# Kernel tuning notes

Measured on AMD Instinct MI355X. Metric: run time of the kernel, lower is better.

## Reference

```python
import jax, jax.numpy as jnp
import numpy as np

SAMPLE_RATE = 16000
SOUND_SPEED = 343.0
MAX_ORDER = 15
RIR_LENGTH = 3968
WINDOW_LENGTH = 81
PAD = WINDOW_LENGTH // 2  # 40

# Static image-source lattice (depends only on max_order): all integer
# reflection index triplets with |nx|+|ny|+|nz| <= max_order.
_ind = np.arange(-MAX_ORDER, MAX_ORDER + 1)
_grid = np.stack(np.meshgrid(_ind, _ind, _ind, indexing="ij"), -1).reshape(-1, 3)
XYZ = _grid[np.abs(_grid).sum(1) <= MAX_ORDER].astype(np.float32)  # (I,3), I=4991
EXP_LO = np.abs(np.floor(XYZ / 2)).astype(np.float32)        # hits on lower walls per dim
EXP_HI = np.abs(np.floor((XYZ + 1) / 2)).astype(np.float32)  # hits on upper walls per dim


def _hann(x, T):
    # continuous Hann window sampled at non-integer points, zero outside |x|<=T/2
    return jnp.where(jnp.abs(x) <= T / 2, 0.5 * (1.0 + jnp.cos(2.0 * jnp.pi * x / T)), 0.0)


def _forward(inp):
    room = inp[:, 0:3]                 # (B,3) room dimensions [m]
    mic = inp[:, 3:6] * room           # (B,3)
    src = inp[:, 6:9] * room           # (B,3)
    a_w = inp[:, 9:10]
    absorption = jnp.concatenate([a_w, a_w, a_w, a_w, inp[:, 10:11], inp[:, 11:12]], axis=1)
    absorption = absorption * 0.84 + 0.01            # (B,6): [x-,x+,y-,y+,floor,ceiling]
    tr = jnp.sqrt(1.0 - absorption)                  # wall reflection coefficients

    xyz = jnp.asarray(XYZ)                           # (I,3)
    d = room[:, None, :]
    s = src[:, None, :]
    # image source locations (B,I,3): mirror parity per torchaudio ISM
    img_loc = jnp.where(xyz % 2 == 1, d * (xyz + 1.0) - s, d * xyz + s)
    # per-image-source attenuation (B,I)
    t_lo = tr[:, None, 0::2]                         # (B,1,3) lower walls per dim
    t_hi = tr[:, None, 1::2]                         # (B,1,3) upper walls per dim
    att = jnp.prod(t_lo ** jnp.asarray(EXP_LO) * t_hi ** jnp.asarray(EXP_HI), axis=-1)

    dist = jnp.linalg.norm(img_loc - mic[:, None, :], axis=-1)   # (B,I)
    amp = att / dist                                              # 1/r spreading
    delay = dist * (SAMPLE_RATE / SOUND_SPEED)                    # fractional sample delay
    delay_i = jnp.ceil(delay)

    # windowed-sinc fractional-delay pulse sampled at n = delay_i-PAD .. delay_i+PAD
    n_rel = jnp.arange(-PAD, PAD + 1, dtype=jnp.float32)          # (W,)
    x = delay_i[..., None] + n_rel - delay[..., None]             # (B,I,W)
    sig = amp[..., None] * jnp.sinc(x) * _hann(x, 2 * PAD)        # (B,I,W)

    # scatter-accumulate pulses at time index n, dropping out-of-range samples
    t_idx = (delay_i[..., None] + n_rel).astype(jnp.int32)        # (B,I,W)
    B = inp.shape[0]
    b_idx = jnp.arange(B, dtype=jnp.int32)[:, None, None]
    rir = jnp.zeros((B, RIR_LENGTH), dtype=sig.dtype).at[b_idx, t_idx].add(sig, mode="drop")

    toa = PAD + SAMPLE_RATE * jnp.linalg.norm(mic - src, axis=1) / SOUND_SPEED  # (B,)
    return rir, toa


def setup_inputs():
    key = jax.random.key(0)
    u = jax.random.uniform(key, (128, 12), dtype=jnp.float32)
    room = 2.0 + 8.0 * u[:, :3]          # room dims in [2,10] m
    rest = 0.05 + 0.9 * u[:, 3:]         # mic/src fractions and absorptions in (0,1)
    return {"input": jnp.concatenate([room, rest], axis=1)}


def reference(input):
    return _forward(input)
```

## Files before the change

### kernel.cpp

```cpp
#include <hip/hip_runtime.h>

#define NIMG    4991
#define RIRLEN  3968
#define NT      512
#define NGRP    16
#define CAP     2048
#define KPT     10
#define INV_PI  0.31830988618379067f
#define SR_OVER_C 46.647230320699704f

struct Tab { int v[NIMG]; };
static constexpr Tab make_tab() {
    Tab t{};
    int k = 0;
    for (int x = -15; x <= 15; ++x)
        for (int y = -15; y <= 15; ++y)
            for (int z = -15; z <= 15; ++z) {
                int ax = x < 0 ? -x : x;
                int ay = y < 0 ? -y : y;
                int az = z < 0 ? -z : z;
                if (ax + ay + az <= 15)
                    t.v[k++] = (x + 15) | ((y + 15) << 8) | ((z + 15) << 16);
            }
    return t;
}
__constant__ Tab c_tab = make_tab();

static __device__ __forceinline__ int iabs(int v) { return v < 0 ? -v : v; }
static __device__ __forceinline__ int imin(int a, int b) { return a < b ? a : b; }

typedef __fp16 f16x2 __attribute__((ext_vector_type(2)));

__global__ __launch_bounds__(NT, 8)
void rir_fused(const float* __restrict__ inp, float* __restrict__ out, int B) {
    const int bx   = blockIdx.x;
    const int b    = bx >> 4;
    const int g    = bx & 15;
    const int tid  = threadIdx.x;
    const int lane = tid & 63;
    const int wv   = tid >> 6;
    const int q    = lane & 3;

    __shared__ __align__(16) float2   s_dh[CAP];
    __shared__ __align__(16) unsigned s_cs[CAP];
    __shared__ float    s_par[12];
    __shared__ float    s_p2[3][32];
    __shared__ float    s_at[3][32];
    __shared__ int      s_h4[256][4];
    __shared__ int      s_off[257];
    __shared__ float    s_acc[4][64];

    for (int k = tid; k < 1024; k += NT) ((int*)s_h4)[k] = 0;
    if (tid < 256) ((float*)s_acc)[tid] = 0.0f;
    if (tid == 0) {
        const float* ip = inp + b * 12;
        float rx = ip[0], ry = ip[1], rz = ip[2];
        float mx = ip[3] * rx, my = ip[4] * ry, mz = ip[5] * rz;
        float sx = ip[6] * rx, sy = ip[7] * ry, sz = ip[8] * rz;
        float aw = __builtin_fmaf(ip[9],  0.84f, 0.01f);
        float a4 = __builtin_fmaf(ip[10], 0.84f, 0.01f);
        float a5 = __builtin_fmaf(ip[11], 0.84f, 0.01f);
        s_par[0] = rx; s_par[1] = ry; s_par[2] = rz;
        s_par[3] = mx; s_par[4] = my; s_par[5] = mz;
        s_par[6] = sx; s_par[7] = sy; s_par[8] = sz;
        s_par[9]  = 0.5f * __builtin_amdgcn_logf(1.0f - aw);
        s_par[10] = 0.5f * __builtin_amdgcn_logf(1.0f - a4);
        s_par[11] = 0.5f * __builtin_amdgcn_logf(1.0f - a5);
        if (g == 0) {
            float dx = mx - sx, dy = my - sy, dz = mz - sz;
            out[(size_t)B * RIRLEN + b] = __builtin_fmaf(
                __builtin_sqrtf(dx * dx + dy * dy + dz * dz), SR_OVER_C, 40.0f);
        }
    }
    __syncthreads();

    if (tid < 96) {
        const int axis = tid >> 5;
        const int j    = tid & 31;
        if (j < 31) {
            const int n = j - 15;
            const float rr = s_par[axis];
            const float mm = s_par[3 + axis];
            const float ss = s_par[6 + axis];
            const float iv = (n & 1) ? __builtin_fmaf(rr, (float)(n + 1), -ss)
                                     : __builtin_fmaf(rr, (float)n, ss);
            const float pv = iv - mm;
            s_p2[axis][j] = pv * pv;
            const float e4 = (float)iabs(n >> 1);
            const float e5 = (float)iabs((n + 1) >> 1);
            const float ex = (axis < 2)
                ? (e4 + e5) * s_par[9]
                : __builtin_fmaf(e4, s_par[10], e5 * s_par[11]);
            s_at[axis][j] = __builtin_amdgcn_exp2f(ex);
        }
    }
    __syncthreads();

    const int fb = 4 * g + 1;

    float2   edh[KPT];
    unsigned ecs[KPT];
    int      enc[KPT];
    #pragma unroll
    for (int k = 0; k < KPT; ++k) {
        enc[k] = -1;
        const int idx = tid + k * NT;
        if (idx < NIMG) {
            const int p  = c_tab.v[idx];
            const int xi = p & 255;
            const int yi = (p >> 8) & 255;
            const int zi = (p >> 16) & 255;
            const float d2   = s_p2[0][xi] + s_p2[1][yi] + s_p2[2][zi];
            const float dist = __builtin_sqrtf(d2);
            const float delay = dist * SR_OVER_C;
            const float di    = __builtin_ceilf(delay);
            const int   ti0   = (int)di - 40;
            const int   bk    = (ti0 + 96) >> 4;
            const bool owned  = ((unsigned)((bk - fb + 64) & 63) < 9u);
            if (ti0 < RIRLEN && owned) {
                const float att = s_at[0][xi] * s_at[1][yi] * s_at[2][zi];
                const float amp = att * __builtin_amdgcn_rcpf(dist);
                float frac = di - delay;
                if (frac == 0.0f) frac = di * 1.52587890625e-05f;
                const int dii = (int)di;
                float c1p = amp * __builtin_amdgcn_sinf(0.5f * frac) * INV_PI;
                if (dii & 1) c1p = -c1p;
                const float Hp     = 0.5f * c1p;
                const float dstore = di - frac;
                const float rv = dstore * 0.0125f;
                const float fr = rv - __builtin_floorf(rv);
                const float Hcd = Hp * __builtin_amdgcn_cosf(fr);
                const float Hsd = Hp * __builtin_amdgcn_sinf(fr);
                const f16x2 pk2 = __builtin_amdgcn_cvt_pkrtz(Hcd, Hsd);

                const int rnk = atomicAdd(&s_h4[bk][q], 1);
                enc[k] = (bk << 13) | rnk;
                edh[k] = make_float2(dstore, Hp);
                ecs[k] = __builtin_bit_cast(unsigned, pk2);
            }
        }
    }
    __syncthreads();

    if (wv == 0) {
        const int l = lane;
        const int4 a0 = *(const int4*)&s_h4[4 * l + 0][0];
        const int4 a1 = *(const int4*)&s_h4[4 * l + 1][0];
        const int4 a2 = *(const int4*)&s_h4[4 * l + 2][0];
        const int4 a3 = *(const int4*)&s_h4[4 * l + 3][0];
        const int c0 = a0.x + a0.y + a0.z + a0.w;
        const int c1 = a1.x + a1.y + a1.z + a1.w;
        const int c2 = a2.x + a2.y + a2.z + a2.w;
        const int c3 = a3.x + a3.y + a3.z + a3.w;
        const int ts = c0 + c1 + c2 + c3;
        int incl = ts;
        #pragma unroll
        for (int d = 1; d < 64; d <<= 1) {
            const int u = __shfl_up(incl, d, 64);
            if (l >= d) incl += u;
        }
        const int base = incl - ts;
        s_off[4 * l + 0] = imin(base, CAP);
        s_off[4 * l + 1] = imin(base + c0, CAP);
        s_off[4 * l + 2] = imin(base + c0 + c1, CAP);
        s_off[4 * l + 3] = imin(base + c0 + c1 + c2, CAP);
        if (l == 63) s_off[256] = imin(incl, CAP);
    }
    __syncthreads();

    if (tid < 256) {
        int run = s_off[tid];
        #pragma unroll
        for (int p = 0; p < 4; ++p) {
            const int c = s_h4[tid][p];
            s_h4[tid][p] = run;
            run += c;
        }
    }
    __syncthreads();

    #pragma unroll
    for (int k = 0; k < KPT; ++k) {
        if (enc[k] >= 0) {
            const int bk   = enc[k] >> 13;
            const int slot = s_h4[bk][q] + (enc[k] & 8191);
            if (slot < CAP) {
                s_dh[slot] = edh[k];
                s_cs[slot] = ecs[k];
            }
        }
    }
    __syncthreads();

    int wlo[4], wlen[4], wpre[4];
    int T = 0, nw = 0;
    #pragma unroll
    for (int kk = 0; kk < 4; ++kk) {
        const int wi = g + 16 * kk;
        wpre[kk] = T;
        if (wi < 62) {
            wlo[kk]  = s_off[4 * wi + 1];
            wlen[kk] = s_off[4 * wi + 10] - wlo[kk];
            T += wlen[kk];
            nw = kk + 1;
        } else { wlo[kk] = 0; wlen[kk] = 0; }
    }
    const int a0r = (T * wv) >> 3;
    const int a1r = (T * (wv + 1)) >> 3;

#define EV1(ACC, DLY, HPV, PKU) do {                                         \
        const f16x2 hh = __builtin_bit_cast(f16x2, (PKU));                   \
        const float xw = tf - (DLY);                                         \
        const float pre = __builtin_fmaf(cth0, (float)hh.x,                  \
                              __builtin_fmaf(sth0, (float)hh.y, (HPV)));     \
        const float hm = (__builtin_fabsf(xw) <= 40.0f) ? pre : 0.0f;        \
        ACC = __builtin_fmaf(hm, __builtin_amdgcn_rcpf(xw), ACC);            \
    } while (0)

    #pragma unroll
    for (int kk = 0; kk < 4; ++kk) {
        if (wlen[kk] == 0) continue;
        const int o0 = (wpre[kk] > a0r) ? wpre[kk] : a0r;
        const int oe = ((wpre[kk] + wlen[kk]) < a1r) ? (wpre[kk] + wlen[kk]) : a1r;
        if (o0 >= oe) continue;
        int       i  = wlo[kk] + (o0 - wpre[kk]);
        const int ie = wlo[kk] + (oe - wpre[kk]);

        const int   wi   = g + 16 * kk;
        const int   t    = (wi << 6) + lane;
        const float tf   = (float)t;
        const int   m    = t - (t / 80) * 80;
        const float cth0 = __builtin_amdgcn_cosf((float)m * 0.0125f);
        const float sth0 = __builtin_amdgcn_sinf((float)m * 0.0125f);

        float acc0 = 0.0f, acc1 = 0.0f;
        while (i < ie && (i & 3)) { EV1(acc0, s_dh[i].x, s_dh[i].y, s_cs[i]); ++i; }
        for (; i + 4 <= ie; i += 4) {
            const float4 d0 = *(const float4*)&s_dh[i];
            const float4 d1 = *(const float4*)&s_dh[i + 2];
            const uint4  cc = *(const uint4*)&s_cs[i];
            EV1(acc0, d0.x, d0.y, cc.x); EV1(acc1, d0.z, d0.w, cc.y);
            EV1(acc0, d1.x, d1.y, cc.z); EV1(acc1, d1.z, d1.w, cc.w);
        }
        for (; i < ie; ++i) EV1(acc0, s_dh[i].x, s_dh[i].y, s_cs[i]);

        atomicAdd(&s_acc[kk][lane], acc0 + acc1);
    }
#undef EV1
    __syncthreads();

    if (tid < 64 * nw) {
        const int kk = tid >> 6;
        const int wi = g + 16 * kk;
        const int t  = (wi << 6) + lane;
        const float sl = (lane & 1) ? -1.0f : 1.0f;
        out[(size_t)b * RIRLEN + t] = sl * s_acc[kk][lane];
    }
}

extern "C" void kernel_launch(void* const* d_in, const int* in_sizes, int n_in,
                              void* d_out, int out_size, void* d_ws, size_t ws_size,
                              hipStream_t stream) {
    (void)d_ws; (void)ws_size; (void)n_in; (void)out_size;
    const float* inp = (const float*)d_in[0];
    float* out = (float*)d_out;
    const int B = in_sizes[0] / 12;
    rir_fused<<<dim3(B * NGRP), dim3(NT), 0, stream>>>(inp, out, B);
}
```

Measured before the change: 103.1 us.

## Split fused RIR kernel into per-batch prep and per-group gather kernels

The fused kernel had each of 16 groups per batch item recompute all ~5000 image sources, bin them and prefix-sum them, keeping only the ones it owns. The new path runs a prep kernel once per batch item that computes, bins and writes sorted image-source data plus offsets to workspace. A gather kernel then loads each group's slice into shared memory and evaluates the windowed-sinc sum. This removes the 16x redundant source computation but adds a second launch and a global-memory round trip. It falls back to the fused kernel when the workspace is too small.

```diff
diff --git a/kernel.cpp b/kernel.cpp
--- a/kernel.cpp
+++ b/kernel.cpp
@@ -28,8 +28,259 @@
 
 static __device__ __forceinline__ int iabs(int v) { return v < 0 ? -v : v; }
 static __device__ __forceinline__ int imin(int a, int b) { return a < b ? a : b; }
+static __device__ __forceinline__ int imax(int a, int b) { return a > b ? a : b; }
 
 typedef __fp16 f16x2 __attribute__((ext_vector_type(2)));
+
+
+__global__ __launch_bounds__(NT)
+void rir_prep(const float* __restrict__ inp, float* __restrict__ out,
+              float2* __restrict__ wdh, unsigned* __restrict__ wcs,
+              int* __restrict__ offs, int B) {
+    const int b    = blockIdx.x;
+    const int tid  = threadIdx.x;
+    const int lane = tid & 63;
+    const int wv   = tid >> 6;
+    const int q    = lane & 3;
+
+    __shared__ float s_par[12];
+    __shared__ float s_p2[3][32];
+    __shared__ float s_at[3][32];
+    __shared__ int   s_h4[256][4];
+    __shared__ int   s_off[257];
+
+    for (int k = tid; k < 1024; k += NT) ((int*)s_h4)[k] = 0;
+    if (tid == 0) {
+        const float* ip = inp + b * 12;
+        float rx = ip[0], ry = ip[1], rz = ip[2];
+        float mx = ip[3] * rx, my = ip[4] * ry, mz = ip[5] * rz;
+        float sx = ip[6] * rx, sy = ip[7] * ry, sz = ip[8] * rz;
+        float aw = __builtin_fmaf(ip[9],  0.84f, 0.01f);
+        float a4 = __builtin_fmaf(ip[10], 0.84f, 0.01f);
+        float a5 = __builtin_fmaf(ip[11], 0.84f, 0.01f);
+        s_par[0] = rx; s_par[1] = ry; s_par[2] = rz;
+        s_par[3] = mx; s_par[4] = my; s_par[5] = mz;
+        s_par[6] = sx; s_par[7] = sy; s_par[8] = sz;
+        s_par[9]  = 0.5f * __builtin_amdgcn_logf(1.0f - aw);
+        s_par[10] = 0.5f * __builtin_amdgcn_logf(1.0f - a4);
+        s_par[11] = 0.5f * __builtin_amdgcn_logf(1.0f - a5);
+        float dx = mx - sx, dy = my - sy, dz = mz - sz;
+        out[(size_t)B * RIRLEN + b] = __builtin_fmaf(
+            __builtin_sqrtf(dx * dx + dy * dy + dz * dz), SR_OVER_C, 40.0f);
+    }
+    __syncthreads();
+
+    if (tid < 96) {
+        const int axis = tid >> 5;
+        const int j    = tid & 31;
+        if (j < 31) {
+            const int n = j - 15;
+            const float rr = s_par[axis];
+            const float mm = s_par[3 + axis];
+            const float ss = s_par[6 + axis];
+            const float iv = (n & 1) ? __builtin_fmaf(rr, (float)(n + 1), -ss)
+                                     : __builtin_fmaf(rr, (float)n, ss);
+            const float pv = iv - mm;
+            s_p2[axis][j] = pv * pv;
+            const float e4 = (float)iabs(n >> 1);
+            const float e5 = (float)iabs((n + 1) >> 1);
+            const float ex = (axis < 2)
+                ? (e4 + e5) * s_par[9]
+                : __builtin_fmaf(e4, s_par[10], e5 * s_par[11]);
+            s_at[axis][j] = __builtin_amdgcn_exp2f(ex);
+        }
+    }
+    __syncthreads();
+
+    float2   edh[KPT];
+    unsigned ecs[KPT];
+    int      enc[KPT];
+    #pragma unroll
+    for (int k = 0; k < KPT; ++k) {
+        enc[k] = -1;
+        const int idx = tid + k * NT;
+        if (idx < NIMG) {
+            const int p  = c_tab.v[idx];
+            const int xi = p & 255;
+            const int yi = (p >> 8) & 255;
+            const int zi = (p >> 16) & 255;
+            const float d2   = s_p2[0][xi] + s_p2[1][yi] + s_p2[2][zi];
+            const float dist = __builtin_sqrtf(d2);
+            const float delay = dist * SR_OVER_C;
+            const float di    = __builtin_ceilf(delay);
+            const int   ti0   = (int)di - 40;
+            if (ti0 < RIRLEN) {
+                const int bk = (ti0 + 96) >> 4;
+                const float att = s_at[0][xi] * s_at[1][yi] * s_at[2][zi];
+                const float amp = att * __builtin_amdgcn_rcpf(dist);
+                float frac = di - delay;
+                if (frac == 0.0f) frac = di * 1.52587890625e-05f;
+                const int dii = (int)di;
+                float c1p = amp * __builtin_amdgcn_sinf(0.5f * frac) * INV_PI;
+                if (dii & 1) c1p = -c1p;
+                const float Hp     = 0.5f * c1p;
+                const float dstore = di - frac;
+                const float rv = dstore * 0.0125f;
+                const float fr = rv - __builtin_floorf(rv);
+                const float Hcd = Hp * __builtin_amdgcn_cosf(fr);
+                const float Hsd = Hp * __builtin_amdgcn_sinf(fr);
+                const f16x2 pk2 = __builtin_amdgcn_cvt_pkrtz(Hcd, Hsd);
+
+                const int rnk = atomicAdd(&s_h4[bk][q], 1);
+                enc[k] = (bk << 13) | rnk;
+                edh[k] = make_float2(dstore, Hp);
+                ecs[k] = __builtin_bit_cast(unsigned, pk2);
+            }
+        }
+    }
+    __syncthreads();
+
+    if (wv == 0) {
+        const int l = lane;
+        const int4 a0 = *(const int4*)&s_h4[4 * l + 0][0];
+        const int4 a1 = *(const int4*)&s_h4[4 * l + 1][0];
+        const int4 a2 = *(const int4*)&s_h4[4 * l + 2][0];
+        const int4 a3 = *(const int4*)&s_h4[4 * l + 3][0];
+        const int c0 = a0.x + a0.y + a0.z + a0.w;
+        const int c1 = a1.x + a1.y + a1.z + a1.w;
+        const int c2 = a2.x + a2.y + a2.z + a2.w;
+        const int c3 = a3.x + a3.y + a3.z + a3.w;
+        const int ts = c0 + c1 + c2 + c3;
+        int incl = ts;
+        #pragma unroll
+        for (int d = 1; d < 64; d <<= 1) {
+            const int u = __shfl_up(incl, d, 64);
+            if (l >= d) incl += u;
+        }
+        const int base = incl - ts;
+        s_off[4 * l + 0] = base;
+        s_off[4 * l + 1] = base + c0;
+        s_off[4 * l + 2] = base + c0 + c1;
+        s_off[4 * l + 3] = base + c0 + c1 + c2;
+        if (l == 63) s_off[256] = incl;
+    }
+    __syncthreads();
+
+    if (tid < 256) {
+        int run = s_off[tid];
+        #pragma unroll
+        for (int p = 0; p < 4; ++p) {
+            const int c = s_h4[tid][p];
+            s_h4[tid][p] = run;
+            run += c;
+        }
+    }
+    __syncthreads();
+
+    float2*   db = wdh + (size_t)b * NIMG;
+    unsigned* cb = wcs + (size_t)b * NIMG;
+    #pragma unroll
+    for (int k = 0; k < KPT; ++k) {
+        if (enc[k] >= 0) {
+            const int bk   = enc[k] >> 13;
+            const int slot = s_h4[bk][q] + (enc[k] & 8191);
+            db[slot] = edh[k];
+            cb[slot] = ecs[k];
+        }
+    }
+    if (tid < 257) offs[b * 257 + tid] = s_off[tid];
+}
+
+__global__ __launch_bounds__(NT, 8)
+void rir_gather(const float2* __restrict__ wdh, const unsigned* __restrict__ wcs,
+                const int* __restrict__ offs, float* __restrict__ out, int B) {
+    const int bx   = blockIdx.x;
+    const int b    = bx >> 4;
+    const int g    = bx & 15;
+    const int tid  = threadIdx.x;
+    const int lane = tid & 63;
+    const int wv   = tid >> 6;
+
+    __shared__ __align__(16) float2   s_dh[CAP];
+    __shared__ __align__(16) unsigned s_cs[CAP];
+    __shared__ float s_acc[4][64];
+
+    if (tid < 256) ((float*)s_acc)[tid] = 0.0f;
+
+    const int* ob = offs + b * 257;
+    int wlo[4], wlen[4], wpre[4];
+    int T = 0, nw = 0;
+    #pragma unroll
+    for (int kk = 0; kk < 4; ++kk) {
+        const int wi = g + 16 * kk;
+        wpre[kk] = T;
+        if (wi < 62) {
+            wlo[kk] = ob[4 * wi + 1];
+            int len = ob[4 * wi + 10] - wlo[kk];
+            if (T + len > CAP) len = CAP - T;
+            if (len < 0) len = 0;
+            wlen[kk] = len;
+            T += len;
+            nw = kk + 1;
+        } else { wlo[kk] = 0; wlen[kk] = 0; }
+    }
+
+    const float2*   db = wdh + (size_t)b * NIMG;
+    const unsigned* cb = wcs + (size_t)b * NIMG;
+    for (int j = tid; j < T; j += NT) {
+        const int kk = (j >= wpre[1] ? 1 : 0) + (j >= wpre[2] ? 1 : 0)
+                     + (j >= wpre[3] ? 1 : 0);
+        const int src = wlo[kk] + (j - wpre[kk]);
+        s_dh[j] = db[src];
+        s_cs[j] = cb[src];
+    }
+    __syncthreads();
+
+    const int a0r = (T * wv) >> 3;
+    const int a1r = (T * (wv + 1)) >> 3;
+
+#define EV1(ACC, DLY, HPV, PKU) do {                                         \
+        const f16x2 hh = __builtin_bit_cast(f16x2, (PKU));                   \
+        const float xw = tf - (DLY);                                         \
+        const float pre = __builtin_fmaf(cth0, (float)hh.x,                  \
+                              __builtin_fmaf(sth0, (float)hh.y, (HPV)));     \
+        const float hm = (__builtin_fabsf(xw) <= 40.0f) ? pre : 0.0f;        \
+        ACC = __builtin_fmaf(hm, __builtin_amdgcn_rcpf(xw), ACC);            \
+    } while (0)
+
+    #pragma unroll
+    for (int kk = 0; kk < 4; ++kk) {
+        if (wlen[kk] == 0) continue;
+        int       i  = imax(wpre[kk], a0r);
+        const int ie = imin(wpre[kk] + wlen[kk], a1r);
+        if (i >= ie) continue;
+
+        const int   wi   = g + 16 * kk;
+        const int   t    = (wi << 6) + lane;
+        const float tf   = (float)t;
+        const int   m    = t - (t / 80) * 80;
+        const float cth0 = __builtin_amdgcn_cosf((float)m * 0.0125f);
+        const float sth0 = __builtin_amdgcn_sinf((float)m * 0.0125f);
+
+        float acc0 = 0.0f, acc1 = 0.0f;
+        while (i < ie && (i & 3)) { EV1(acc0, s_dh[i].x, s_dh[i].y, s_cs[i]); ++i; }
+        for (; i + 4 <= ie; i += 4) {
+            const float4 d0 = *(const float4*)&s_dh[i];
+            const float4 d1 = *(const float4*)&s_dh[i + 2];
+            const uint4  cc = *(const uint4*)&s_cs[i];
+            EV1(acc0, d0.x, d0.y, cc.x); EV1(acc1, d0.z, d0.w, cc.y);
+            EV1(acc0, d1.x, d1.y, cc.z); EV1(acc1, d1.z, d1.w, cc.w);
+        }
+        for (; i < ie; ++i) EV1(acc0, s_dh[i].x, s_dh[i].y, s_cs[i]);
+
+        atomicAdd(&s_acc[kk][lane], acc0 + acc1);
+    }
+#undef EV1
+    __syncthreads();
+
+    if (tid < 64 * nw) {
+        const int kk = tid >> 6;
+        const int wi = g + 16 * kk;
+        const int t  = (wi << 6) + lane;
+        const float sl = (lane & 1) ? -1.0f : 1.0f;
+        out[(size_t)b * RIRLEN + t] = sl * s_acc[kk][lane];
+    }
+}
 
 __global__ __launch_bounds__(NT, 8)
 void rir_fused(const float* __restrict__ inp, float* __restrict__ out, int B) {
@@ -132,7 +383,6 @@
                 const float Hcd = Hp * __builtin_amdgcn_cosf(fr);
                 const float Hsd = Hp * __builtin_amdgcn_sinf(fr);
                 const f16x2 pk2 = __builtin_amdgcn_cvt_pkrtz(Hcd, Hsd);
-
                 const int rnk = atomicAdd(&s_h4[bk][q], 1);
                 enc[k] = (bk << 13) | rnk;
                 edh[k] = make_float2(dstore, Hp);
@@ -220,8 +470,8 @@
     #pragma unroll
     for (int kk = 0; kk < 4; ++kk) {
         if (wlen[kk] == 0) continue;
-        const int o0 = (wpre[kk] > a0r) ? wpre[kk] : a0r;
-        const int oe = ((wpre[kk] + wlen[kk]) < a1r) ? (wpre[kk] + wlen[kk]) : a1r;
+        const int o0 = imax(wpre[kk], a0r);
+        const int oe = imin(wpre[kk] + wlen[kk], a1r);
         if (o0 >= oe) continue;
         int       i  = wlo[kk] + (o0 - wpre[kk]);
         const int ie = wlo[kk] + (oe - wpre[kk]);
@@ -261,9 +511,24 @@
 extern "C" void kernel_launch(void* const* d_in, const int* in_sizes, int n_in,
                               void* d_out, int out_size, void* d_ws, size_t ws_size,
                               hipStream_t stream) {
-    (void)d_ws; (void)ws_size; (void)n_in; (void)out_size;
+    (void)n_in; (void)out_size;
     const float* inp = (const float*)d_in[0];
     float* out = (float*)d_out;
     const int B = in_sizes[0] / 12;
-    rir_fused<<<dim3(B * NGRP), dim3(NT), 0, stream>>>(inp, out, B);
+
+    const size_t dh_bytes   = (size_t)B * NIMG * sizeof(float2);
+    const size_t cs_bytes   = (size_t)B * NIMG * sizeof(unsigned);
+    const size_t offs_bytes = (size_t)B * 257 * sizeof(int);
+    const int use_ws = (d_ws != nullptr &&
+                        ws_size >= dh_bytes + cs_bytes + offs_bytes) ? 1 : 0;
+
+    if (use_ws) {
+        float2*   wdh  = (float2*)d_ws;
+        unsigned* wcs  = (unsigned*)((char*)d_ws + dh_bytes);
+        int*      offs = (int*)((char*)d_ws + dh_bytes + cs_bytes);
+        rir_prep  <<<dim3(B),        dim3(NT), 0, stream>>>(inp, out, wdh, wcs, offs, B);
+        rir_gather<<<dim3(B * NGRP), dim3(NT), 0, stream>>>(wdh, wcs, offs, out, B);
+    } else {
+        rir_fused<<<dim3(B * NGRP), dim3(NT), 0, stream>>>(inp, out, B);
+    }
 }
```

Result: faster. 100.8 us (-2.3%).
